# Optimization experiments

Hardware: AMD Instinct MI355X
Metric: run time of the kernel (lower is better)

## Reference

```python
import jax, jax.numpy as jnp
import numpy as np

D_MODEL, N_HEADS, N_GROUPS, BASE = 2048, 32, 8, 10000
HEAD_DIM = D_MODEL // N_HEADS  # 64


def _rope_cache(seq, head_dim, base=BASE):
    half = head_dim // 2
    theta = 1.0 / (base ** (jnp.arange(0, head_dim, 2)[:half].astype(jnp.float32) / head_dim))
    ang = jnp.einsum('i,j->ij', jnp.arange(seq, dtype=jnp.float32), theta)  # (seq, half)
    return jnp.cos(ang), jnp.sin(ang)


def _apply_rope(x):
    # x: (b, s, h, head_dim) -> interleaved-pair rotation, matching torch module
    b, s, h, hd = x.shape
    cos, sin = _rope_cache(s, hd)
    xr = x.reshape(b, s, h, hd // 2, 2)
    c = cos[None, :, None, :]
    sn = sin[None, :, None, :]
    x0, x1 = xr[..., 0], xr[..., 1]
    out = jnp.stack((x0 * c - x1 * sn, x1 * c + x0 * sn), axis=-1)
    return out.reshape(b, s, h, hd).astype(x.dtype)


def setup_inputs() -> dict:
    key = jax.random.key(0)
    ks = jax.random.split(key, 8)
    B, S = 1, 2048
    kv_dim = HEAD_DIM * N_GROUPS
    return {
        'Q': jax.random.normal(ks[0], (B, S, D_MODEL), jnp.float32),
        'K': jax.random.normal(ks[1], (B, S, D_MODEL), jnp.float32),
        'V': jax.random.normal(ks[2], (B, S, D_MODEL), jnp.float32),
        'attention_mask': jnp.ones((B, S), jnp.int32),
        'Wq': jax.random.normal(ks[3], (D_MODEL, D_MODEL), jnp.float32) * 0.02,
        'Wk': jax.random.normal(ks[4], (D_MODEL, kv_dim), jnp.float32) * 0.02,
        'Wv': jax.random.normal(ks[5], (D_MODEL, kv_dim), jnp.float32) * 0.02,
        'Wo': jax.random.normal(ks[6], (D_MODEL, D_MODEL), jnp.float32) * 0.02,
        'bo': jnp.zeros((D_MODEL,), jnp.float32),
    }


def reference(Q, K, V, attention_mask, Wq, Wk, Wv, Wo, bo):
    b, s, _ = Q.shape
    g, hpg, hd = N_GROUPS, N_HEADS // N_GROUPS, HEAD_DIM
    # projections (weights stored as [in, out], equivalent to torch x @ W.T)
    q = (Q @ Wq).reshape(b, s, N_HEADS, hd)
    q = _apply_rope(q).reshape(b, s, g, hpg, hd)
    k = _apply_rope((K @ Wk).reshape(b, s, g, hd))
    v = (V @ Wv).reshape(b, s, g, hd)

    scale = jnp.sqrt(jnp.float32(hd))
    scores = jnp.einsum('bnghd,bmgd->bnghm', q, k) / scale  # (b, s, g, hpg, s)
    # padding mask (b, 1, 1, 1, s) and causal mask (1, s, 1, 1, s)
    pad = (attention_mask != 0)[:, None, None, None, :]
    causal = jnp.tril(jnp.ones((s, s), bool))[None, :, None, None, :]
    scores = jnp.where(pad & causal, scores, -jnp.inf)
    attn = jax.nn.softmax(scores, axis=-1)  # dropout p=0.0 -> identity
    out = jnp.einsum('bnghm,bmgd->bnghd', attn, v).reshape(b, s, D_MODEL)
    return out @ Wo + bo
```

## Files before the change

kernel.cpp:

```cpp
#include <hip/hip_runtime.h>

typedef __bf16 bf16_t;
typedef __bf16 bf16x8 __attribute__((ext_vector_type(8)));
typedef __bf16 bf16x4 __attribute__((ext_vector_type(4)));
typedef __bf16 bf16x2 __attribute__((ext_vector_type(2)));
typedef float  f32x4  __attribute__((ext_vector_type(4)));

#define LOG2E 1.44269504088896340736f

#define GLDS(gp, lp)                                                           \
  __builtin_amdgcn_global_load_lds(                                            \
      (const __attribute__((address_space(1))) void*)(gp),                     \
      (__attribute__((address_space(3))) void*)(lp), 16, 0, 0)

__global__ __launch_bounds__(256) void rope_table_k(float* __restrict__ cs,
                                                    float* __restrict__ sn, int S) {
  int i = blockIdx.x * 256 + threadIdx.x;
  if (i >= S * 32) return;
  int s = i >> 5, j = i & 31;
  float theta = powf(10000.0f, -(float)j * (1.0f / 32.0f));
  float a = (float)s * theta;
  cs[i] = cosf(a);
  sn[i] = sinf(a);
}

__global__ __launch_bounds__(256) void cast3_k(const float* __restrict__ A,
                                               const float* __restrict__ B,
                                               const float* __restrict__ C,
                                               bf16_t* __restrict__ oa,
                                               bf16_t* __restrict__ ob,
                                               bf16_t* __restrict__ oc) {
  const int b = blockIdx.x;
  const float* in; bf16_t* out;
  if (b < 2048) { in = A; out = oa; }
  else if (b < 4096) { in = B; out = ob; }
  else { in = C; out = oc; }
  const int j = (b & 2047) * 256 + threadIdx.x;
  const float4 v0 = *(const float4*)&in[(size_t)j * 8];
  const float4 v1 = *(const float4*)&in[(size_t)j * 8 + 4];
  bf16x8 o;
  o[0]=(bf16_t)v0.x; o[1]=(bf16_t)v0.y; o[2]=(bf16_t)v0.z; o[3]=(bf16_t)v0.w;
  o[4]=(bf16_t)v1.x; o[5]=(bf16_t)v1.y; o[6]=(bf16_t)v1.z; o[7]=(bf16_t)v1.w;
  *(bf16x8*)&out[(size_t)j * 8] = o;
}

__global__ void transpose4_k(const float* __restrict__ Wq, const float* __restrict__ Wk,
                             const float* __restrict__ Wv, const float* __restrict__ Wo,
                             bf16_t* __restrict__ WqT, bf16_t* __restrict__ WkT,
                             bf16_t* __restrict__ WvT, bf16_t* __restrict__ WoT) {
  __shared__ float tile[32][33];
  const int bx = blockIdx.x;
  const float* in; bf16_t* out; int C, cbl;
  if (bx < 64)      { in = Wq; out = WqT; C = 2048; cbl = bx; }
  else if (bx < 80) { in = Wk; out = WkT; C = 512;  cbl = bx - 64; }
  else if (bx < 96) { in = Wv; out = WvT; C = 512;  cbl = bx - 80; }
  else              { in = Wo; out = WoT; C = 2048; cbl = bx - 96; }
  const int R = 2048;
  int c0 = cbl * 32, r0 = blockIdx.y * 32;
  int tx = threadIdx.x, ty = threadIdx.y;
  #pragma unroll
  for (int k = 0; k < 32; k += 8)
    tile[ty + k][tx] = in[(size_t)(r0 + ty + k) * C + c0 + tx];
  __syncthreads();
  #pragma unroll
  for (int k = 0; k < 32; k += 8)
    out[(size_t)(c0 + ty + k) * R + r0 + tx] = (bf16_t)tile[tx][ty + k];
}

__device__ __forceinline__ int xcd_swz(int bid, int nb) {
  const int q = nb >> 3;
  return (bid & 7) * q + (bid >> 3);
}
__device__ __forceinline__ void st_map(int lin, int nstc, int& rb, int& cb) {
  const int stid = lin >> 4, w = lin & 15;
  const int sr = stid / nstc, t = stid - sr * nstc;
  const int sc = (sr & 1) ? (nstc - 1 - t) : t;
  rb = sr * 4 + (w >> 2);
  cb = sc * 4 + (w & 3);
}

template<int MODE>
__global__ __launch_bounds__(256) void gemm_glds_k(
    const bf16_t* __restrict__ Aq, const bf16_t* __restrict__ Ak, const bf16_t* __restrict__ Av,
    const bf16_t* __restrict__ Bq, const bf16_t* __restrict__ Bk, const bf16_t* __restrict__ Bv,
    const int K, const float* __restrict__ cs, const float* __restrict__ sn,
    bf16_t* __restrict__ oq, bf16_t* __restrict__ okg, bf16_t* __restrict__ ovt,
    float* __restrict__ ofp, const float* __restrict__ bias, const int S) {
  __shared__ bf16_t a_lds[64 * 64];
  __shared__ bf16_t b_lds[128 * 64];
  const int tid = threadIdx.x, wid = tid >> 6, lane = tid & 63;
  const int fr = lane & 15, kg = lane >> 4;

  constexpr int NB   = (MODE == 0) ? 768 : 512;
  constexpr int NSTC = (MODE == 0) ? 6 : 4;
  const int lin = xcd_swz(blockIdx.x, NB);
  int rb, cb; st_map(lin, NSTC, rb, cb);
  const bf16_t* Ap; const bf16_t* Bp; int emode, col0;
  if (MODE == 1)    { Ap = Aq; Bp = Bq; emode = 3; col0 = cb * 128; }
  else if (cb < 16) { Ap = Aq; Bp = Bq; emode = 0; col0 = cb * 128; }
  else if (cb < 20) { Ap = Ak; Bp = Bk; emode = 1; col0 = (cb - 16) * 128; }
  else              { Ap = Av; Bp = Bv; emode = 2; col0 = (cb - 20) * 128; }
  const int row0 = rb * 64;
  const int wr = (wid >> 1) * 32, wc = (wid & 1) * 64;

  f32x4 acc[2][4];
  #pragma unroll
  for (int i = 0; i < 2; ++i)
    #pragma unroll
    for (int j = 0; j < 4; ++j)
      acc[i][j] = (f32x4){0.f, 0.f, 0.f, 0.f};

  const int rloc = lane >> 3;
  const int schunk = ((lane & 7) ^ rloc) * 8;
  const bf16_t* gA0 = Ap + (size_t)(row0 + (wid * 2 + 0) * 8 + rloc) * K + schunk;
  const bf16_t* gA1 = Ap + (size_t)(row0 + (wid * 2 + 1) * 8 + rloc) * K + schunk;
  const bf16_t* gB0 = Bp + (size_t)(col0 + (wid * 4 + 0) * 8 + rloc) * K + schunk;
  const bf16_t* gB1 = Bp + (size_t)(col0 + (wid * 4 + 1) * 8 + rloc) * K + schunk;
  const bf16_t* gB2 = Bp + (size_t)(col0 + (wid * 4 + 2) * 8 + rloc) * K + schunk;
  const bf16_t* gB3 = Bp + (size_t)(col0 + (wid * 4 + 3) * 8 + rloc) * K + schunk;
  bf16_t* lA0 = &a_lds[(wid * 2 + 0) * 512];
  bf16_t* lA1 = &a_lds[(wid * 2 + 1) * 512];
  bf16_t* lB0 = &b_lds[(wid * 4 + 0) * 512];
  bf16_t* lB1 = &b_lds[(wid * 4 + 1) * 512];
  bf16_t* lB2 = &b_lds[(wid * 4 + 2) * 512];
  bf16_t* lB3 = &b_lds[(wid * 4 + 3) * 512];

  for (int kt = 0; kt < K; kt += 64) {
    __syncthreads();
    GLDS(gA0 + kt, lA0);
    GLDS(gA1 + kt, lA1);
    GLDS(gB0 + kt, lB0);
    GLDS(gB1 + kt, lB1);
    GLDS(gB2 + kt, lB2);
    GLDS(gB3 + kt, lB3);
    __syncthreads();
    #pragma unroll
    for (int ks = 0; ks < 2; ++ks) {
      bf16x8 af[2], bfr[4];
      #pragma unroll
      for (int mi = 0; mi < 2; ++mi) {
        const int r = wr + mi * 16 + fr;
        af[mi] = *(const bf16x8*)&a_lds[r * 64 + (((ks * 4 + kg) ^ (fr & 7)) * 8)];
      }
      #pragma unroll
      for (int ni = 0; ni < 4; ++ni) {
        const int r = wc + ni * 16 + fr;
        bfr[ni] = *(const bf16x8*)&b_lds[r * 64 + (((ks * 4 + kg) ^ (fr & 7)) * 8)];
      }
      #pragma unroll
      for (int mi = 0; mi < 2; ++mi)
        #pragma unroll
        for (int ni = 0; ni < 4; ++ni)
          acc[mi][ni] = __builtin_amdgcn_mfma_f32_16x16x32_bf16(af[mi], bfr[ni], acc[mi][ni], 0, 0, 0);
    }
  }

  #pragma unroll
  for (int mi = 0; mi < 2; ++mi) {
    #pragma unroll
    for (int ni = 0; ni < 4; ++ni) {
      #pragma unroll
      for (int r = 0; r < 4; ++r) {
        const int grow = row0 + wr + mi * 16 + kg * 4 + r;
        const int gcol = col0 + wc + ni * 16 + fr;
        float v = acc[mi][ni][r];
        if (emode == 3) {
          ofp[(size_t)grow * 2048 + gcol] = v + bias[gcol];
        } else if (emode == 2) {
          const int gi = gcol >> 6, d = gcol & 63;
          ovt[((size_t)gi * 64 + d) * S + grow] = (bf16_t)v;
        } else {
          const float pv = __shfl_xor(v, 1);
          const int d = gcol & 63, p = d >> 1, hh = gcol >> 6;
          const float c = cs[grow * 32 + p], s = sn[grow * 32 + p];
          float o = (d & 1) ? fmaf(pv, s, v * c) : fmaf(-pv, s, v * c);
          if (emode == 0) {
            o *= 0.125f * LOG2E;
            oq[((size_t)hh * S + grow) * 64 + d] = (bf16_t)o;
          } else {
            okg[((size_t)hh * S + grow) * 64 + d] = (bf16_t)o;
          }
        }
      }
    }
  }
}

__device__ __forceinline__ int swz8(int r, int c) { return r * 64 + (((c) ^ (r & 7)) << 3); }

__global__ __launch_bounds__(256) void attn_k(
    const bf16_t* __restrict__ qh,
    const bf16_t* __restrict__ kgr,
    const bf16_t* __restrict__ vtg,
    const int* __restrict__ amask,
    bf16_t* __restrict__ ao,
    const int S) {
  __shared__ bf16_t k_lds[64 * 64];
  __shared__ bf16_t vt_lds[64 * 64];
  __shared__ bf16_t p_lds[4][16 * 64];
  const int tid = threadIdx.x, wid = tid >> 6, lane = tid & 63;
  const int fr = lane & 15, kgp = lane >> 4;
  const int h = blockIdx.x, g = h >> 2;
  const int qb = 31 - blockIdx.y;
  const int q0 = qb * 64 + wid * 16;
  const int qg = q0 + fr;

  const bf16_t* qbase = qh + ((size_t)h * S + q0 + fr) * 64;
  const bf16x8 qf0 = *(const bf16x8*)&qbase[kgp * 8];
  const bf16x8 qf1 = *(const bf16x8*)&qbase[32 + kgp * 8];

  f32x4 oacc[4];
  #pragma unroll
  for (int t = 0; t < 4; ++t) oacc[t] = (f32x4){0.f, 0.f, 0.f, 0.f};
  float m_ = -1e30f, l_ = 0.f;

  const int srow = tid >> 2, sc4 = tid & 3;
  const bf16_t* kbase = kgr + (size_t)g * S * 64;
  const bf16_t* vbase = vtg + (size_t)g * 64 * S;
  const int cmax = qb + 1;

  bf16x8 nk0 = *(const bf16x8*)&kbase[(size_t)srow * 64 + sc4 * 8];
  bf16x8 nk1 = *(const bf16x8*)&kbase[(size_t)srow * 64 + 32 + sc4 * 8];
  bf16x8 nv0 = *(const bf16x8*)&vbase[(size_t)srow * S + sc4 * 8];
  bf16x8 nv1 = *(const bf16x8*)&vbase[(size_t)srow * S + 32 + sc4 * 8];
  int mvc = amask[lane];
  *(bf16x8*)&k_lds[swz8(srow, sc4)]      = nk0;
  *(bf16x8*)&k_lds[swz8(srow, 4 + sc4)]  = nk1;
  *(bf16x8*)&vt_lds[swz8(srow, sc4)]     = nv0;
  *(bf16x8*)&vt_lds[swz8(srow, 4 + sc4)] = nv1;
  __syncthreads();

  for (int c = 0; c < cmax; ++c) {
    const int kc0 = c * 64;
    const unsigned long long pm = __ballot(mvc == 0);
    const bool more = (c + 1 < cmax);
    if (more) {
      const int kc1 = kc0 + 64;
      nk0 = *(const bf16x8*)&kbase[(size_t)(kc1 + srow) * 64 + sc4 * 8];
      nk1 = *(const bf16x8*)&kbase[(size_t)(kc1 + srow) * 64 + 32 + sc4 * 8];
      nv0 = *(const bf16x8*)&vbase[(size_t)srow * S + kc1 + sc4 * 8];
      nv1 = *(const bf16x8*)&vbase[(size_t)srow * S + kc1 + 32 + sc4 * 8];
      mvc = amask[kc1 + lane];
    }

    f32x4 sc[4];
    #pragma unroll
    for (int a = 0; a < 4; ++a) {
      const bf16x8 ka0 = *(const bf16x8*)&k_lds[swz8(a * 16 + fr, kgp)];
      const bf16x8 ka1 = *(const bf16x8*)&k_lds[swz8(a * 16 + fr, 4 + kgp)];
      f32x4 z = (f32x4){0.f, 0.f, 0.f, 0.f};
      z = __builtin_amdgcn_mfma_f32_16x16x32_bf16(ka0, qf0, z, 0, 0, 0);
      z = __builtin_amdgcn_mfma_f32_16x16x32_bf16(ka1, qf1, z, 0, 0, 0);
      sc[a] = z;
    }

    if (c == qb) {
      #pragma unroll
      for (int a = 0; a < 4; ++a)
        #pragma unroll
        for (int r = 0; r < 4; ++r) {
          const int kl = a * 16 + 4 * kgp + r;
          if (kc0 + kl > qg) sc[a][r] = -1e30f;
        }
    }
    if (pm) {
      #pragma unroll
      for (int a = 0; a < 4; ++a)
        #pragma unroll
        for (int r = 0; r < 4; ++r) {
          const int kl = a * 16 + 4 * kgp + r;
          if ((pm >> kl) & 1) sc[a][r] = -1e30f;
        }
    }

    float t0 = fmaxf(fmaxf(sc[0][0], sc[0][1]), fmaxf(sc[0][2], sc[0][3]));
    float t1 = fmaxf(fmaxf(sc[1][0], sc[1][1]), fmaxf(sc[1][2], sc[1][3]));
    float t2 = fmaxf(fmaxf(sc[2][0], sc[2][1]), fmaxf(sc[2][2], sc[2][3]));
    float t3 = fmaxf(fmaxf(sc[3][0], sc[3][1]), fmaxf(sc[3][2], sc[3][3]));
    float smax = fmaxf(fmaxf(t0, t1), fmaxf(t2, t3));
    smax = fmaxf(smax, __shfl_xor(smax, 16));
    smax = fmaxf(smax, __shfl_xor(smax, 32));

    const bool rescale = !__all(smax <= m_ + 8.0f);
    if (rescale) {
      const float mn = fmaxf(m_, smax);
      const float al = exp2f(m_ - mn);
      m_ = mn;
      #pragma unroll
      for (int t = 0; t < 4; ++t)
        #pragma unroll
        for (int r = 0; r < 4; ++r) oacc[t][r] *= al;
      l_ *= al;
    }

    float ps = 0.f;
    #pragma unroll
    for (int a = 0; a < 4; ++a)
      #pragma unroll
      for (int r = 0; r < 4; ++r) {
        const float p = exp2f(sc[a][r] - m_);
        sc[a][r] = p;
        ps += p;
      }
    ps += __shfl_xor(ps, 16);
    ps += __shfl_xor(ps, 32);
    l_ += ps;

    #pragma unroll
    for (int a = 0; a < 4; ++a) {
      bf16x4 w;
      w[0] = (bf16_t)sc[a][0];
      w[1] = (bf16_t)sc[a][1];
      w[2] = (bf16_t)sc[a][2];
      w[3] = (bf16_t)sc[a][3];
      const int off = a * 16 + 4 * kgp;
      *(bf16x4*)&p_lds[wid][fr * 64 + (((off >> 3) ^ (fr & 7)) << 3) + (off & 7)] = w;
    }
    const bf16x8 pa0 = *(const bf16x8*)&p_lds[wid][swz8(fr, kgp)];
    const bf16x8 pa1 = *(const bf16x8*)&p_lds[wid][swz8(fr, 4 + kgp)];

    #pragma unroll
    for (int t = 0; t < 4; ++t) {
      const bf16x8 vb0 = *(const bf16x8*)&vt_lds[swz8(t * 16 + fr, kgp)];
      const bf16x8 vb1 = *(const bf16x8*)&vt_lds[swz8(t * 16 + fr, 4 + kgp)];
      oacc[t] = __builtin_amdgcn_mfma_f32_16x16x32_bf16(vb0, pa0, oacc[t], 0, 0, 0);
      oacc[t] = __builtin_amdgcn_mfma_f32_16x16x32_bf16(vb1, pa1, oacc[t], 0, 0, 0);
    }

    if (more) {
      __syncthreads();
      *(bf16x8*)&k_lds[swz8(srow, sc4)]      = nk0;
      *(bf16x8*)&k_lds[swz8(srow, 4 + sc4)]  = nk1;
      *(bf16x8*)&vt_lds[swz8(srow, sc4)]     = nv0;
      *(bf16x8*)&vt_lds[swz8(srow, 4 + sc4)] = nv1;
      __syncthreads();
    }
  }

  const float inv = 1.0f / l_;
  #pragma unroll
  for (int t = 0; t < 4; ++t) {
    bf16x4 o4;
    #pragma unroll
    for (int r = 0; r < 4; ++r) o4[r] = (bf16_t)(oacc[t][r] * inv);
    *(bf16x4*)&ao[(size_t)(q0 + fr) * 2048 + h * 64 + t * 16 + 4 * kgp] = o4;
  }
}

extern "C" void kernel_launch(void* const* d_in, const int* in_sizes, int n_in,
                              void* d_out, int out_size, void* d_ws, size_t ws_size,
                              hipStream_t stream) {
  const float* Q  = (const float*)d_in[0];
  const float* K  = (const float*)d_in[1];
  const float* V  = (const float*)d_in[2];
  const int*   am = (const int*)d_in[3];
  const float* Wq = (const float*)d_in[4];
  const float* Wk = (const float*)d_in[5];
  const float* Wv = (const float*)d_in[6];
  const float* Wo = (const float*)d_in[7];
  const float* bo = (const float*)d_in[8];
  float* out = (float*)d_out;

  const int S = 2048, D = 2048;
  char* w = (char*)d_ws;
  const size_t MB = 1u << 20;
  bf16_t* WqT = (bf16_t*)(w + 0 * MB);
  bf16_t* WoT = (bf16_t*)(w + 8 * MB);
  bf16_t* WkT = (bf16_t*)(w + 16 * MB);
  bf16_t* WvT = (bf16_t*)(w + 18 * MB);
  bf16_t* qh  = (bf16_t*)(w + 20 * MB);
  bf16_t* kgr = (bf16_t*)(w + 28 * MB);
  bf16_t* vtg = (bf16_t*)(w + 30 * MB);
  bf16_t* ao  = (bf16_t*)(w + 32 * MB);
  bf16_t* Qb  = (bf16_t*)(w + 40 * MB);
  bf16_t* Kb  = (bf16_t*)(w + 48 * MB);
  bf16_t* Vb  = (bf16_t*)(w + 56 * MB);
  float*  cs  = (float*)(w + 64 * MB);
  float*  sn  = (float*)(w + 64 * MB + 256 * 1024);

  rope_table_k<<<256, 256, 0, stream>>>(cs, sn, S);
  cast3_k<<<6144, 256, 0, stream>>>(Q, K, V, Qb, Kb, Vb);
  transpose4_k<<<dim3(160, 64), dim3(32, 8), 0, stream>>>(Wq, Wk, Wv, Wo, WqT, WkT, WvT, WoT);

  gemm_glds_k<0><<<768, 256, 0, stream>>>(Qb, Kb, Vb, WqT, WkT, WvT, D,
                                          cs, sn, qh, kgr, vtg, nullptr, nullptr, S);

  attn_k<<<dim3(32, 32), 256, 0, stream>>>(qh, kgr, vtg, am, ao, S);

  gemm_glds_k<1><<<512, 256, 0, stream>>>(ao, nullptr, nullptr, WoT, nullptr, nullptr,
                                          D, nullptr, nullptr, nullptr, nullptr, nullptr,
                                          out, bo, S);
}
```

Measured before the change: 152.0 us.

## Split long causal query blocks across two KV halves with a merge kernel

New measurement: 162.8 us. +7.1%, slower.

```diff
diff --git a/kernel.cpp b/kernel.cpp
--- a/kernel.cpp
+++ b/kernel.cpp
@@ -194,6 +194,8 @@
     const bf16_t* __restrict__ vtg,
     const int* __restrict__ amask,
     bf16_t* __restrict__ ao,
+    float* __restrict__ opart,
+    float* __restrict__ lm,
     const int S) {
   __shared__ bf16_t k_lds[64 * 64];
   __shared__ bf16_t vt_lds[64 * 64];
@@ -201,7 +203,21 @@
   const int tid = threadIdx.x, wid = tid >> 6, lane = tid & 63;
   const int fr = lane & 15, kgp = lane >> 4;
   const int h = blockIdx.x, g = h >> 2;
-  const int qb = 31 - blockIdx.y;
+  const int y = blockIdx.y;
+  int qb, cbeg, cend, half; bool split;
+  if (y < 32) {
+    const int p = y >> 1;
+    qb = 31 - p;
+    half = y & 1;
+    const int n = qb + 1, nh = n >> 1;
+    cbeg = half ? nh : 0;
+    cend = half ? n : nh;
+    split = true;
+  } else {
+    qb = 47 - y;
+    half = 0; cbeg = 0; cend = qb + 1;
+    split = false;
+  }
   const int q0 = qb * 64 + wid * 16;
   const int qg = q0 + fr;
 
@@ -217,23 +233,23 @@
   const int srow = tid >> 2, sc4 = tid & 3;
   const bf16_t* kbase = kgr + (size_t)g * S * 64;
   const bf16_t* vbase = vtg + (size_t)g * 64 * S;
-  const int cmax = qb + 1;
-
-  bf16x8 nk0 = *(const bf16x8*)&kbase[(size_t)srow * 64 + sc4 * 8];
-  bf16x8 nk1 = *(const bf16x8*)&kbase[(size_t)srow * 64 + 32 + sc4 * 8];
-  bf16x8 nv0 = *(const bf16x8*)&vbase[(size_t)srow * S + sc4 * 8];
-  bf16x8 nv1 = *(const bf16x8*)&vbase[(size_t)srow * S + 32 + sc4 * 8];
-  int mvc = amask[lane];
+
+  const int kb0 = cbeg * 64;
+  bf16x8 nk0 = *(const bf16x8*)&kbase[(size_t)(kb0 + srow) * 64 + sc4 * 8];
+  bf16x8 nk1 = *(const bf16x8*)&kbase[(size_t)(kb0 + srow) * 64 + 32 + sc4 * 8];
+  bf16x8 nv0 = *(const bf16x8*)&vbase[(size_t)srow * S + kb0 + sc4 * 8];
+  bf16x8 nv1 = *(const bf16x8*)&vbase[(size_t)srow * S + kb0 + 32 + sc4 * 8];
+  int mvc = amask[kb0 + lane];
   *(bf16x8*)&k_lds[swz8(srow, sc4)]      = nk0;
   *(bf16x8*)&k_lds[swz8(srow, 4 + sc4)]  = nk1;
   *(bf16x8*)&vt_lds[swz8(srow, sc4)]     = nv0;
   *(bf16x8*)&vt_lds[swz8(srow, 4 + sc4)] = nv1;
   __syncthreads();
 
-  for (int c = 0; c < cmax; ++c) {
+  for (int c = cbeg; c < cend; ++c) {
     const int kc0 = c * 64;
     const unsigned long long pm = __ballot(mvc == 0);
-    const bool more = (c + 1 < cmax);
+    const bool more = (c + 1 < cend);
     if (more) {
       const int kc1 = kc0 + 64;
       nk0 = *(const bf16x8*)&kbase[(size_t)(kc1 + srow) * 64 + sc4 * 8];
@@ -337,13 +353,53 @@
     }
   }
 
-  const float inv = 1.0f / l_;
-  #pragma unroll
-  for (int t = 0; t < 4; ++t) {
-    bf16x4 o4;
-    #pragma unroll
-    for (int r = 0; r < 4; ++r) o4[r] = (bf16_t)(oacc[t][r] * inv);
-    *(bf16x4*)&ao[(size_t)(q0 + fr) * 2048 + h * 64 + t * 16 + 4 * kgp] = o4;
+  if (!split) {
+    const float inv = 1.0f / l_;
+    #pragma unroll
+    for (int t = 0; t < 4; ++t) {
+      bf16x4 o4;
+      #pragma unroll
+      for (int r = 0; r < 4; ++r) o4[r] = (bf16_t)(oacc[t][r] * inv);
+      *(bf16x4*)&ao[(size_t)(q0 + fr) * 2048 + h * 64 + t * 16 + 4 * kgp] = o4;
+    }
+  } else {
+    const int idx = ((qb - 16) * 32 + h) * 2 + half;
+    float* op = opart + (size_t)idx * 4096;
+    const int qr = wid * 16 + fr;
+    #pragma unroll
+    for (int t = 0; t < 4; ++t)
+      *(f32x4*)&op[qr * 64 + t * 16 + 4 * kgp] = oacc[t];
+    if (kgp == 0) {
+      lm[(size_t)idx * 128 + qr] = l_;
+      lm[(size_t)idx * 128 + 64 + qr] = m_;
+    }
+  }
+}
+
+__global__ __launch_bounds__(256) void attn_merge_k(
+    const float* __restrict__ opart, const float* __restrict__ lm,
+    bf16_t* __restrict__ ao) {
+  const int b = blockIdx.x;
+  const int qbp = b >> 5, h = b & 31;
+  const int t = threadIdx.x;
+  const int row = t >> 2, ds = (t & 3) * 16;
+  const size_t i0 = (size_t)(qbp * 32 + h) * 2;
+  const float l0 = lm[i0 * 128 + row],       m0 = lm[i0 * 128 + 64 + row];
+  const float l1 = lm[(i0 + 1) * 128 + row], m1 = lm[(i0 + 1) * 128 + 64 + row];
+  const float m = fmaxf(m0, m1);
+  const float a0 = exp2f(m0 - m), a1 = exp2f(m1 - m);
+  const float inv = 1.0f / (l0 * a0 + l1 * a1);
+  const float* p0 = opart + i0 * 4096 + row * 64 + ds;
+  const float* p1 = opart + (i0 + 1) * 4096 + row * 64 + ds;
+  bf16_t* dst = ao + (size_t)((qbp + 16) * 64 + row) * 2048 + h * 64 + ds;
+  #pragma unroll
+  for (int j = 0; j < 16; j += 4) {
+    const f32x4 v0 = *(const f32x4*)(p0 + j);
+    const f32x4 v1 = *(const f32x4*)(p1 + j);
+    bf16x4 o;
+    #pragma unroll
+    for (int r = 0; r < 4; ++r) o[r] = (bf16_t)((v0[r] * a0 + v1[r] * a1) * inv);
+    *(bf16x4*)(dst + j) = o;
   }
 }
 
@@ -375,6 +431,8 @@
   bf16_t* Qb  = (bf16_t*)(w + 40 * MB);
   bf16_t* Kb  = (bf16_t*)(w + 48 * MB);
   bf16_t* Vb  = (bf16_t*)(w + 56 * MB);
+  float* opart = (float*)(w + 40 * MB);
+  float* lmw   = (float*)(w + 56 * MB);
   float*  cs  = (float*)(w + 64 * MB);
   float*  sn  = (float*)(w + 64 * MB + 256 * 1024);
 
@@ -385,7 +443,8 @@
   gemm_glds_k<0><<<768, 256, 0, stream>>>(Qb, Kb, Vb, WqT, WkT, WvT, D,
                                           cs, sn, qh, kgr, vtg, nullptr, nullptr, S);
 
-  attn_k<<<dim3(32, 32), 256, 0, stream>>>(qh, kgr, vtg, am, ao, S);
+  attn_k<<<dim3(32, 48), 256, 0, stream>>>(qh, kgr, vtg, am, ao, opart, lmw, S);
+  attn_merge_k<<<512, 256, 0, stream>>>(opart, lmw, ao);
 
   gemm_glds_k<1><<<512, 256, 0, stream>>>(ao, nullptr, nullptr, WoT, nullptr, nullptr,
                                           D, nullptr, nullptr, nullptr, nullptr, nullptr,
```
